# Kernel optimization log

Hardware: AMD Instinct MI355X
Metric: run time of the kernel (lower is better)

Reference implementation:

```python
import jax, jax.numpy as jnp
from jax import lax
import numpy as np

B, S, G = 16, 384, 384
N = S + G
E_CHAR, D = 100, 128
H = D // 2              # LSTM hidden per direction
NHEAD, NHID = 4, 64
T = 21                  # crf_input_dim = label_alphabet.size() + 1
START, STOP = T - 2, T - 1
ALPHA = 0.2
CHAR_V, GAZ_V = 8000, 100000
NEG = -9e15             # pyGAT masked_fill value


def setup_inputs():
    key = jax.random.key(0)
    ks = jax.random.split(key, 20)
    f32 = jnp.float32
    def nrm(k, shape, s=0.05):
        return (jax.random.normal(k, shape) * s).astype(f32)
    eye = jnp.eye(N, dtype=bool)
    def adj(k):
        return ((jax.random.uniform(k, (B, N, N)) < 0.1) | eye[None]).astype(jnp.int32)
    return dict(
        batch_char=jax.random.randint(ks[0], (B, S), 0, CHAR_V),
        batch_len=jnp.full((B,), S, jnp.int32),
        gaz_list=jax.random.randint(ks[1], (B, G), 0, GAZ_V),
        t_graph=adj(ks[2]), c_graph=adj(ks[3]), l_graph=adj(ks[4]),
        mask=jnp.ones((B, S), jnp.int32),
        char_table=nrm(ks[5], (CHAR_V, E_CHAR)),
        gaz_table=nrm(ks[6], (GAZ_V, D)),
        w_ih_f=nrm(ks[7], (4 * H, E_CHAR)), w_hh_f=nrm(ks[8], (4 * H, H)),
        b_f=jnp.zeros((4 * H,), f32),
        w_ih_b=nrm(ks[9], (4 * H, E_CHAR)), w_hh_b=nrm(ks[10], (4 * H, H)),
        b_b=jnp.zeros((4 * H,), f32),
        h2h_W=nrm(ks[11], (T, D)), h2h_b=jnp.zeros((T,), f32),
        gat_Wh=nrm(ks[12], (3, NHEAD, D, NHID)),
        gat_ah=nrm(ks[13], (3, NHEAD, 2 * NHID)),
        gat_Wo=nrm(ks[14], (3, NHEAD * NHID, T)),
        gat_ao=nrm(ks[15], (3, 2 * T)),
        fuse_w=jnp.ones((4,), f32),
        transitions=nrm(ks[16], (T, T)),
    )


def _lstm_dir(x, w_ih, w_hh, b, reverse):
    # x: [B,S,E]; torch gate order i,f,g,o
    Bb = x.shape[0]
    Hh = w_hh.shape[1]
    xw = jnp.einsum('bse,ge->bsg', x, w_ih) + b
    def step(carry, xt):
        h, c = carry
        g = xt + h @ w_hh.T
        i, f, gg, o = jnp.split(g, 4, axis=-1)
        c = jax.nn.sigmoid(f) * c + jax.nn.sigmoid(i) * jnp.tanh(gg)
        h = jax.nn.sigmoid(o) * jnp.tanh(c)
        return (h, c), h
    h0 = jnp.zeros((Bb, Hh), x.dtype)
    _, hs = lax.scan(step, (h0, h0), xw.swapaxes(0, 1), reverse=reverse)
    return hs.swapaxes(0, 1)


def _gat_layer(x, adj, W, a, concat):
    # pyGAT batched layer: e_ij = LeakyReLU(a . [Wh_i || Wh_j]), masked softmax over j
    h = jnp.einsum('bnd,df->bnf', x, W)
    F_ = W.shape[1]
    f1 = h @ a[:F_]           # [B,N]
    f2 = h @ a[F_:]
    e = jax.nn.leaky_relu(f1[:, :, None] + f2[:, None, :], negative_slope=ALPHA)
    e = jnp.where(adj > 0, e, NEG)
    att = jax.nn.softmax(e, axis=-1)
    out = jnp.einsum('bij,bjf->bif', att, h)
    return jax.nn.elu(out) if concat else out


def _gat(x, adj, Wh, ah, Wo, ao):
    heads = jax.vmap(lambda W, a: _gat_layer(x, adj, W, a, True))(Wh, ah)  # [H,B,N,F]
    hcat = jnp.moveaxis(heads, 0, 2).reshape(x.shape[0], x.shape[1], -1)
    return jax.nn.elu(_gat_layer(hcat, adj, Wo, ao, False))


def _crf_feature(batch_char, gaz_list, graphs, char_table, gaz_table,
                 w_ih_f, w_hh_f, b_f, w_ih_b, w_hh_b, b_b, h2h_W, h2h_b,
                 gat_Wh, gat_ah, gat_Wo, gat_ao, fuse_w):
    emb = char_table[batch_char]                      # [B,S,E_CHAR]
    hf = _lstm_dir(emb, w_ih_f, w_hh_f, b_f, False)
    hb = _lstm_dir(emb, w_ih_b, w_hh_b, b_b, True)
    lstm_feat = jnp.concatenate([hf, hb], axis=-1)    # [B,S,D]
    gaz_feat = gaz_table[gaz_list]                    # [B,G,D]
    gat_in = jnp.concatenate([lstm_feat, gaz_feat], axis=1)  # [B,N,D]
    gat_outs = [_gat(gat_in, adj, gat_Wh[k], gat_ah[k], gat_Wo[k], gat_ao[k])[:, :S]
                for k, adj in enumerate(graphs)]
    lstm_proj = lstm_feat @ h2h_W.T + h2h_b           # [B,S,T]
    return (fuse_w[0] * lstm_proj + fuse_w[1] * gat_outs[0]
            + fuse_w[2] * gat_outs[1] + fuse_w[3] * gat_outs[2])


def _viterbi(feats, transitions, mask):
    Bb, Ss, Tt = feats.shape
    ids = jnp.arange(Tt)
    part0 = feats[:, 0, :] + transitions[START][None, :]
    def step(part, inp):
        feat_t, m_t = inp
        cur = part[:, :, None] + transitions[None] + feat_t[:, None, :]  # [B,prev,cur]
        new = cur.max(axis=1)
        bp = cur.argmax(axis=1)
        m = (m_t > 0)[:, None]
        return jnp.where(m, new, part), jnp.where(m, bp, ids[None, :])
    part, bps = lax.scan(step, part0,
                         (feats[:, 1:].swapaxes(0, 1), mask[:, 1:].swapaxes(0, 1)))
    last_tag = jnp.argmax(part + transitions[:, STOP][None, :], axis=1)
    def back(tag, bp):
        prev = jnp.take_along_axis(bp, tag[:, None], axis=1)[:, 0]
        return prev, prev
    _, prevs = lax.scan(back, last_tag, bps, reverse=True)   # prevs[j] = tag at time j
    return jnp.concatenate([prevs.swapaxes(0, 1), last_tag[:, None]], axis=1)


def reference(batch_char, batch_len, gaz_list, t_graph, c_graph, l_graph, mask,
              char_table, gaz_table, w_ih_f, w_hh_f, b_f, w_ih_b, w_hh_b, b_b,
              h2h_W, h2h_b, gat_Wh, gat_ah, gat_Wo, gat_ao, fuse_w, transitions):
    # batch_len is all == S (mask all ones), so packed BiLSTM == plain BiLSTM
    feats = _crf_feature(batch_char, gaz_list, (t_graph, c_graph, l_graph),
                         char_table, gaz_table, w_ih_f, w_hh_f, b_f,
                         w_ih_b, w_hh_b, b_b, h2h_W, h2h_b,
                         gat_Wh, gat_ah, gat_Wo, gat_ao, fuse_w)
    return _viterbi(feats, transitions, mask)
```

## Files before the change

kernel.cpp:

```cpp
#include <hip/hip_runtime.h>
#include <hip/hip_bf16.h>
#include <cstdint>
#include <cstddef>

#define BB 16
#define SS 384
#define GG 384
#define NN 768
#define DD 128
#define EC 100
#define TT 21
#define NHEADS 4
#define BN (BB*NN)
#define BS (BB*SS)

typedef float v2f __attribute__((ext_vector_type(2)));

__device__ __forceinline__ float sigf(float x) { return 1.0f / (1.0f + __expf(-x)); }
__device__ __forceinline__ float tanh_fast(float x) {
    return 1.0f - 2.0f / (__expf(2.0f * x) + 1.0f);
}
__device__ __forceinline__ float wred_max(float v) {
    #pragma unroll
    for (int o = 32; o > 0; o >>= 1) v = fmaxf(v, __shfl_xor(v, o));
    return v;
}
__device__ __forceinline__ float wred_sum(float v) {
    #pragma unroll
    for (int o = 32; o > 0; o >>= 1) v += __shfl_xor(v, o);
    return v;
}

__global__ __launch_bounds__(256) void k_xw(
    const int* __restrict__ batch_char, const float* __restrict__ char_table,
    const float* __restrict__ w_ih_f, const float* __restrict__ b_f,
    const float* __restrict__ w_ih_b, const float* __restrict__ b_b,
    float* __restrict__ xw_f, float* __restrict__ xw_b)
{
    __shared__ float At[EC * 68];
    __shared__ float Bt[EC * 68];
    __shared__ int   chs[64];
    const int tid = threadIdx.x;
    const int rt  = blockIdx.x;
    const int ot  = blockIdx.y;
    const int dir = ot >> 2, gt = ot & 3;
    const float* wih  = dir ? w_ih_b : w_ih_f;
    const float* bias = dir ? b_b    : b_f;
    float*       out  = dir ? xw_b   : xw_f;

    if (tid < 64) chs[tid] = batch_char[rt * 64 + tid];
    __syncthreads();
    for (int idx = tid; idx < 64 * EC; idx += 256) {
        int r = idx / EC, e = idx - r * EC;
        At[e * 68 + r] = char_table[(size_t)chs[r] * EC + e];
        Bt[e * 68 + r] = wih[(size_t)(gt * 64 + r) * EC + e];
    }
    __syncthreads();

    const int ty = tid >> 4, tx = tid & 15;
    const int r0 = ty * 4, c0 = tx * 4;
    float acc[4][4] = {};
    #pragma unroll 4
    for (int e = 0; e < EC; ++e) {
        float4 a = *(const float4*)&At[e * 68 + r0];
        float4 bv = *(const float4*)&Bt[e * 68 + c0];
        float av[4] = {a.x, a.y, a.z, a.w};
        float bb[4] = {bv.x, bv.y, bv.z, bv.w};
        #pragma unroll
        for (int i = 0; i < 4; ++i)
            #pragma unroll
            for (int j = 0; j < 4; ++j) acc[i][j] = fmaf(av[i], bb[j], acc[i][j]);
    }
    #pragma unroll
    for (int i = 0; i < 4; ++i) {
        int row = rt * 64 + r0 + i;
        int gc  = gt * 64 + c0;
        float4 o;
        o.x = acc[i][0] + bias[gc + 0];
        o.y = acc[i][1] + bias[gc + 1];
        o.z = acc[i][2] + bias[gc + 2];
        o.w = acc[i][3] + bias[gc + 3];
        *(float4*)&out[(size_t)row * 256 + gc] = o;
    }
}

__global__ __launch_bounds__(256) void k_gaz(
    const int* __restrict__ gaz_list, const float* __restrict__ gaz_table,
    float* __restrict__ gat_in)
{
    int idx = blockIdx.x * 256 + threadIdx.x;
    int d = idx & 127;
    int rest = idx >> 7;
    int g = rest % GG;
    int b = rest / GG;
    float v = gaz_table[(size_t)gaz_list[b * GG + g] * DD + d];
    gat_in[((size_t)b * NN + SS + g) * DD + d] = v;
}

__global__ __launch_bounds__(256) void k_lstm(
    const float* __restrict__ xw_f, const float* __restrict__ xw_b,
    const float* __restrict__ w_hh_f, const float* __restrict__ w_hh_b,
    float* __restrict__ gat_in)
{
    __shared__ float part[2][4][64][4];
    __shared__ float hbuf[4][64];
    const int tid = threadIdx.x, wv = tid >> 6, lane = tid & 63;
    const int b = blockIdx.x >> 1, dir = blockIdx.x & 1;
    const float* xw  = (dir ? xw_b : xw_f) + (size_t)b * SS * 256;
    const float* whh = dir ? w_hh_b : w_hh_f;
    v2f w2[4][8];
    #pragma unroll
    for (int g4 = 0; g4 < 4; ++g4) {
        const float* r = whh + (size_t)(g4 * 64 + lane) * 64 + 16 * wv;
        #pragma unroll
        for (int jj = 0; jj < 8; ++jj) w2[g4][jj] = v2f{r[2 * jj], r[2 * jj + 1]};
    }
    hbuf[wv][lane] = 0.f;
    float c = 0.f;
    int buf = 0;
    const int t0 = dir ? (SS - 1) : 0;
    float x0 = xw[t0 * 256 +   0 + lane];
    float x1 = xw[t0 * 256 +  64 + lane];
    float x2 = xw[t0 * 256 + 128 + lane];
    float x3 = xw[t0 * 256 + 192 + lane];
    const v2f* h2p = (const v2f*)&hbuf[wv][16 * wv];
    for (int tt = 0; tt < SS; ++tt) {
        const int t = dir ? (SS - 1 - tt) : tt;
        const int tn = dir ? (t - 1) : (t + 1);
        v2f a0 = v2f{0.f, 0.f}, a1 = v2f{0.f, 0.f}, a2 = v2f{0.f, 0.f}, a3 = v2f{0.f, 0.f};
        #pragma unroll
        for (int jj = 0; jj < 8; ++jj) {
            v2f hv = h2p[jj];
            a0 = __builtin_elementwise_fma(hv, w2[0][jj], a0);
            a1 = __builtin_elementwise_fma(hv, w2[1][jj], a1);
            a2 = __builtin_elementwise_fma(hv, w2[2][jj], a2);
            a3 = __builtin_elementwise_fma(hv, w2[3][jj], a3);
        }
        float4 pw;
        pw.x = a0.x + a0.y; pw.y = a1.x + a1.y;
        pw.z = a2.x + a2.y; pw.w = a3.x + a3.y;
        *(float4*)part[buf][wv][lane] = pw;
        float nx0 = 0.f, nx1 = 0.f, nx2 = 0.f, nx3 = 0.f;
        if (tt + 1 < SS) {
            nx0 = xw[tn * 256 +   0 + lane];
            nx1 = xw[tn * 256 +  64 + lane];
            nx2 = xw[tn * 256 + 128 + lane];
            nx3 = xw[tn * 256 + 192 + lane];
        }
        __syncthreads();
        float4 p0 = *(const float4*)part[buf][0][lane];
        float4 p1 = *(const float4*)part[buf][1][lane];
        float4 p2 = *(const float4*)part[buf][2][lane];
        float4 p3 = *(const float4*)part[buf][3][lane];
        float gi = ((p0.x + p1.x) + (p2.x + p3.x)) + x0;
        float gf = ((p0.y + p1.y) + (p2.y + p3.y)) + x1;
        float gg = ((p0.z + p1.z) + (p2.z + p3.z)) + x2;
        float go = ((p0.w + p1.w) + (p2.w + p3.w)) + x3;
        float nc = sigf(gf) * c + sigf(gi) * tanh_fast(gg);
        float nh = sigf(go) * tanh_fast(nc);
        c = nc;
        hbuf[wv][lane] = nh;
        if (wv == 0) gat_in[((size_t)b * NN + t) * DD + dir * 64 + lane] = nh;
        x0 = nx0; x1 = nx1; x2 = nx2; x3 = nx3;
        buf ^= 1;
    }
}

__global__ __launch_bounds__(256) void k_p1(
    const float* __restrict__ gat_in, const float* __restrict__ gat_Wh,
    const float* __restrict__ gat_ah, int k,
    float* __restrict__ h1, float* __restrict__ f1g, float* __restrict__ f2g)
{
    __shared__ float At[64 * 68];
    __shared__ float Bt[64 * 68];
    __shared__ float sf1[64], sf2[64];
    const int tid = threadIdx.x;
    const int rt = blockIdx.x, hd = blockIdx.y;
    if (tid < 64) { sf1[tid] = 0.f; sf2[tid] = 0.f; }
    const float* W = gat_Wh + ((size_t)(k * NHEADS + hd)) * DD * 64;
    const int ty = tid >> 4, tx = tid & 15;
    const int r0 = ty * 4, c0 = tx * 4;
    float acc[4][4] = {};
    for (int ph = 0; ph < 2; ++ph) {
        __syncthreads();
        for (int idx = tid; idx < 64 * 64; idx += 256) {
            int r = idx >> 6, e = idx & 63;
            At[e * 68 + r] = gat_in[((size_t)(rt * 64 + r)) * DD + ph * 64 + e];
            Bt[e * 68 + r] = W[(size_t)(ph * 64 + e) * 64 + r];
        }
        __syncthreads();
        #pragma unroll 4
        for (int e = 0; e < 64; ++e) {
            float4 a = *(const float4*)&At[e * 68 + r0];
            float4 bv = *(const float4*)&Bt[e * 68 + c0];
            float av[4] = {a.x, a.y, a.z, a.w};
            float bb[4] = {bv.x, bv.y, bv.z, bv.w};
            #pragma unroll
            for (int i = 0; i < 4; ++i)
                #pragma unroll
                for (int j = 0; j < 4; ++j) acc[i][j] = fmaf(av[i], bb[j], acc[i][j]);
        }
    }
    const float* ah = gat_ah + (size_t)(k * NHEADS + hd) * 128;
    float a1[4], a2[4];
    #pragma unroll
    for (int j = 0; j < 4; ++j) { a1[j] = ah[c0 + j]; a2[j] = ah[64 + c0 + j]; }
    #pragma unroll
    for (int i = 0; i < 4; ++i) {
        int n = rt * 64 + r0 + i;
        float4 o = make_float4(acc[i][0], acc[i][1], acc[i][2], acc[i][3]);
        *(float4*)&h1[((size_t)n * NHEADS + hd) * 64 + c0] = o;
        float p1 = acc[i][0] * a1[0] + acc[i][1] * a1[1] + acc[i][2] * a1[2] + acc[i][3] * a1[3];
        float p2 = acc[i][0] * a2[0] + acc[i][1] * a2[1] + acc[i][2] * a2[2] + acc[i][3] * a2[3];
        atomicAdd(&sf1[r0 + i], p1);
        atomicAdd(&sf2[r0 + i], p2);
    }
    __syncthreads();
    if (tid < 64) {
        f1g[hd * BN + rt * 64 + tid] = sf1[tid];
        f2g[hd * BN + rt * 64 + tid] = sf2[tid];
    }
}

__global__ __launch_bounds__(256) void k_attn1(
    const int* __restrict__ adj, const float* __restrict__ h1,
    const float* __restrict__ f1g, const float* __restrict__ f2g,
    float* __restrict__ out1, unsigned long long* __restrict__ packed)
{
    __shared__ int   nbr[NN];
    __shared__ float ep[NHEADS][NN];
    __shared__ unsigned long long wm[12];
    __shared__ int cntS;
    const int tid = threadIdx.x, wave = tid >> 6, lane = tid & 63;
    const int n = blockIdx.x;
    const int b = n / NN;
    #pragma unroll
    for (int it = 0; it < 3; ++it) {
        int j = it * 256 + tid;
        int a = adj[(size_t)n * NN + j];
        unsigned long long m = __ballot(a > 0);
        if (lane == 0) { wm[it * 4 + wave] = m; packed[(size_t)n * 12 + it * 4 + wave] = m; }
    }
    __syncthreads();
    if (wave == 0) {
        unsigned long long m = (lane < 12) ? wm[lane] : 0ULL;
        int pc = __popcll(m);
        int inc = pc;
        #pragma unroll
        for (int d = 1; d < 16; d <<= 1) { int t = __shfl_up(inc, d); if (lane >= d) inc += t; }
        int C = __shfl(inc, 11);
        if (lane == 0) cntS = C;
        int off = inc - pc;
        while (m) {
            int bit = __builtin_ctzll(m);
            nbr[off++] = lane * 64 + bit;
            m &= m - 1;
        }
    }
    __syncthreads();
    const int C = cntS;
    const int hd = wave;
    const float f1 = f1g[hd * BN + n];
    const float* f2p = f2g + hd * BN + b * NN;
    float mx = -3.0e38f;
    for (int t = lane; t < C; t += 64) {
        float e = f1 + f2p[nbr[t]];
        e = (e >= 0.f) ? e : 0.2f * e;
        ep[hd][t] = e;
        mx = fmaxf(mx, e);
    }
    mx = wred_max(mx);
    float sum = 0.f;
    for (int t = lane; t < C; t += 64) {
        float p = __expf(ep[hd][t] - mx);
        ep[hd][t] = p;
        sum += p;
    }
    sum = wred_sum(sum);
    const float* hb = h1 + (size_t)b * NN * (NHEADS * 64) + hd * 64 + lane;
    float ac0 = 0.f, ac1 = 0.f, ac2 = 0.f, ac3 = 0.f;
    int t = 0;
    for (; t + 3 < C; t += 4) {
        int j0 = nbr[t], j1 = nbr[t + 1], j2 = nbr[t + 2], j3 = nbr[t + 3];
        float p0 = ep[hd][t], p1 = ep[hd][t + 1], p2 = ep[hd][t + 2], p3 = ep[hd][t + 3];
        ac0 = fmaf(p0, hb[(size_t)j0 * 256], ac0);
        ac1 = fmaf(p1, hb[(size_t)j1 * 256], ac1);
        ac2 = fmaf(p2, hb[(size_t)j2 * 256], ac2);
        ac3 = fmaf(p3, hb[(size_t)j3 * 256], ac3);
    }
    for (; t < C; ++t) ac0 = fmaf(ep[hd][t], hb[(size_t)nbr[t] * 256], ac0);
    float r = ((ac0 + ac1) + (ac2 + ac3)) / sum;
    r = (r > 0.f) ? r : expm1f(r);
    out1[(size_t)n * 256 + hd * 64 + lane] = r;
}

__global__ __launch_bounds__(256) void k_p2(
    const float* __restrict__ out1, const float* __restrict__ gat_Wo,
    const float* __restrict__ gat_ao, int k,
    float* __restrict__ h2, float* __restrict__ f1o, float* __restrict__ f2o)
{
    __shared__ float ld[12 * 256];
    __shared__ float lf1[12], lf2[12];
    const int tid = threadIdx.x;
    const int blk = blockIdx.x;
    if (tid < 12) { lf1[tid] = 0.f; lf2[tid] = 0.f; }
    for (int idx = tid; idx < 12 * 256; idx += 256)
        ld[idx] = out1[(size_t)blk * 12 * 256 + idx];
    __syncthreads();
    if (tid < 252) {
        const int r = tid / TT, c = tid - r * TT;
        const float* Wo = gat_Wo + (size_t)k * 256 * TT;
        const float4* row4 = (const float4*)&ld[r * 256];
        float acc = 0.f;
        #pragma unroll 8
        for (int q4 = 0; q4 < 64; ++q4) {
            float4 v = row4[q4];
            int q = q4 * 4;
            acc = fmaf(v.x, Wo[(q + 0) * TT + c], acc);
            acc = fmaf(v.y, Wo[(q + 1) * TT + c], acc);
            acc = fmaf(v.z, Wo[(q + 2) * TT + c], acc);
            acc = fmaf(v.w, Wo[(q + 3) * TT + c], acc);
        }
        const int n = blk * 12 + r;
        h2[(size_t)n * TT + c] = acc;
        const float* ao = gat_ao + k * 2 * TT;
        atomicAdd(&lf1[r], acc * ao[c]);
        atomicAdd(&lf2[r], acc * ao[TT + c]);
    }
    __syncthreads();
    if (tid < 12) {
        f1o[blk * 12 + tid] = lf1[tid];
        f2o[blk * 12 + tid] = lf2[tid];
    }
}

__global__ __launch_bounds__(64) void k_attn2(
    const unsigned long long* __restrict__ packed,
    const float* __restrict__ h2, const float* __restrict__ f1o,
    const float* __restrict__ f2o, float* __restrict__ out2k)
{
    __shared__ int   nbr[NN];
    __shared__ float ep[NN];
    const int lane = threadIdx.x;
    const int blk = blockIdx.x;
    const int b = blk / SS, s = blk - b * SS;
    const int n = b * NN + s;
    unsigned long long w64 = (lane < 12) ? packed[(size_t)n * 12 + lane] : 0ULL;
    int pc = __popcll(w64);
    int inc = pc;
    #pragma unroll
    for (int d = 1; d < 16; d <<= 1) {
        int t = __shfl_up(inc, d, 16);
        if ((lane & 15) >= d) inc += t;
    }
    const int C = __shfl(inc, 11);
    int off = inc - pc;
    while (w64) {
        int bit = __builtin_ctzll(w64);
        nbr[off++] = lane * 64 + bit;
        w64 &= w64 - 1;
    }
    __syncthreads();
    const float f1 = f1o[n];
    const float* f2p = f2o + b * NN;
    float mx = -3.0e38f;
    for (int t = lane; t < C; t += 64) {
        int j = nbr[t];
        float e = f1 + f2p[j];
        e = (e >= 0.f) ? e : 0.2f * e;
        ep[t] = e;
        mx = fmaxf(mx, e);
    }
    mx = wred_max(mx);
    float sum = 0.f;
    for (int t = lane; t < C; t += 64) {
        float p = __expf(ep[t] - mx);
        ep[t] = p;
        sum += p;
    }
    sum = wred_sum(sum);
    const float* h2b = h2 + (size_t)b * NN * TT + ((lane < TT) ? lane : 0);
    float ac0 = 0.f, ac1 = 0.f, ac2 = 0.f, ac3 = 0.f;
    int t = 0;
    for (; t + 3 < C; t += 4) {
        int j0 = nbr[t], j1 = nbr[t + 1], j2 = nbr[t + 2], j3 = nbr[t + 3];
        float p0 = ep[t], p1 = ep[t + 1], p2 = ep[t + 2], p3 = ep[t + 3];
        ac0 = fmaf(p0, h2b[(size_t)j0 * TT], ac0);
        ac1 = fmaf(p1, h2b[(size_t)j1 * TT], ac1);
        ac2 = fmaf(p2, h2b[(size_t)j2 * TT], ac2);
        ac3 = fmaf(p3, h2b[(size_t)j3 * TT], ac3);
    }
    for (; t < C; ++t) ac0 = fmaf(ep[t], h2b[(size_t)nbr[t] * TT], ac0);
    if (lane < TT) {
        float r = ((ac0 + ac1) + (ac2 + ac3)) / sum;
        r = (r > 0.f) ? r : expm1f(r);
        out2k[(size_t)blk * TT + lane] = r;
    }
}

__global__ __launch_bounds__(64) void k_fuse(
    const float* __restrict__ gat_in, const float* __restrict__ h2h_W,
    const float* __restrict__ h2h_b, const float* __restrict__ fuse_w,
    const float* __restrict__ out2, float* __restrict__ feats)
{
    __shared__ float row[DD];
    const int lane = threadIdx.x;
    const int blk = blockIdx.x;
    const int b = blk / SS, s = blk - b * SS;
    const float* src = gat_in + ((size_t)b * NN + s) * DD;
    row[lane] = src[lane];
    row[lane + 64] = src[lane + 64];
    __syncthreads();
    if (lane < TT) {
        float acc = h2h_b[lane];
        const float4* w4 = (const float4*)&h2h_W[lane * DD];
        const float4* r4 = (const float4*)row;
        #pragma unroll 8
        for (int d4 = 0; d4 < 32; ++d4) {
            float4 w = w4[d4]; float4 v = r4[d4];
            acc = fmaf(w.x, v.x, acc); acc = fmaf(w.y, v.y, acc);
            acc = fmaf(w.z, v.z, acc); acc = fmaf(w.w, v.w, acc);
        }
        size_t o = (size_t)blk * TT + lane;
        feats[o] = fuse_w[0] * acc + fuse_w[1] * out2[o]
                 + fuse_w[2] * out2[(size_t)BS * TT + o]
                 + fuse_w[3] * out2[2 * (size_t)BS * TT + o];
    }
}

__global__ __launch_bounds__(64) void k_vit(
    const float* __restrict__ feats, const float* __restrict__ trans,
    int* __restrict__ out)
{
    __shared__ float part[24];
    __shared__ unsigned char bp[SS - 1][24];
    const int lane = threadIdx.x;
    const int b = blockIdx.x;
    const int pg = lane / TT;
    const int c = lane - pg * TT;
    const bool act = (pg < 3);
    const int p0 = pg * 7;
    float tc[7];
    if (act) {
        #pragma unroll
        for (int u = 0; u < 7; ++u) tc[u] = trans[(p0 + u) * TT + c];
    }
    if (lane < TT) part[lane] = feats[((size_t)b * SS) * TT + lane] + trans[19 * TT + lane];
    if (lane >= TT && lane < 24) part[lane] = -3.0e38f;
    __syncthreads();
    for (int t = 1; t < SS; ++t) {
        float best = -3.0e38f; int bi = 0;
        if (act) {
            #pragma unroll
            for (int u = 0; u < 7; ++u) {
                float v = part[p0 + u] + tc[u];
                if (v > best) { best = v; bi = p0 + u; }
            }
        }
        float bv1 = __shfl(best, lane + 21);
        int   bi1 = __shfl(bi,   lane + 21);
        float bv2 = __shfl(best, lane + 42);
        int   bi2 = __shfl(bi,   lane + 42);
        if (lane < TT) {
            if (bv1 > best) { best = bv1; bi = bi1; }
            if (bv2 > best) { best = bv2; bi = bi2; }
            bp[t - 1][lane] = (unsigned char)bi;
            part[lane] = best + feats[((size_t)b * SS + t) * TT + lane];
        }
        __syncthreads();
    }
    float fv = (lane < TT) ? part[lane] + trans[lane * TT + 20] : -3.0e38f;
    int fi = (lane < TT) ? lane : 0;
    #pragma unroll
    for (int o = 32; o > 0; o >>= 1) {
        float ov = __shfl_xor(fv, o);
        int oi = __shfl_xor(fi, o);
        if (ov > fv || (ov == fv && oi < fi)) { fv = ov; fi = oi; }
    }
    __syncthreads();
    if (lane == 0) {
        int cur = fi;
        out[b * SS + SS - 1] = cur;
        for (int u = SS - 2; u >= 0; --u) {
            cur = bp[u][cur];
            out[b * SS + u] = cur;
        }
    }
}

extern "C" void kernel_launch(void* const* d_in, const int* in_sizes, int n_in,
                              void* d_out, int out_size, void* d_ws, size_t ws_size,
                              hipStream_t stream) {
    (void)in_sizes; (void)n_in; (void)out_size; (void)ws_size;
    const int*   batch_char = (const int*)d_in[0];
    const int*   gaz_list   = (const int*)d_in[2];
    const int*   graphs[3]  = {(const int*)d_in[3], (const int*)d_in[4], (const int*)d_in[5]};
    const float* char_table = (const float*)d_in[7];
    const float* gaz_table  = (const float*)d_in[8];
    const float* w_ih_f = (const float*)d_in[9];
    const float* w_hh_f = (const float*)d_in[10];
    const float* b_f    = (const float*)d_in[11];
    const float* w_ih_b = (const float*)d_in[12];
    const float* w_hh_b = (const float*)d_in[13];
    const float* b_b    = (const float*)d_in[14];
    const float* h2h_W  = (const float*)d_in[15];
    const float* h2h_b  = (const float*)d_in[16];
    const float* gat_Wh = (const float*)d_in[17];
    const float* gat_ah = (const float*)d_in[18];
    const float* gat_Wo = (const float*)d_in[19];
    const float* gat_ao = (const float*)d_in[20];
    const float* fuse_w = (const float*)d_in[21];
    const float* trans  = (const float*)d_in[22];

    float* ws = (float*)d_ws;
    float* gat_in = ws;
    float* xw_f   = gat_in + 1572864;
    float* xw_b   = xw_f   + 1572864;
    float* h1     = xw_b   + 1572864;
    float* out1   = h1     + 3145728;
    float* h2     = out1   + 3145728;
    float* f1g    = h2     + 258048;
    float* f2g    = f1g    + 49152;
    float* f1o    = f2g    + 49152;
    float* f2o    = f1o    + 12288;
    float* out2   = f2o    + 12288;
    float* feats  = out2   + 387072;
    unsigned long long* packed = (unsigned long long*)(feats + 129024);

    k_xw<<<dim3(96, 8), 256, 0, stream>>>(batch_char, char_table, w_ih_f, b_f,
                                          w_ih_b, b_b, xw_f, xw_b);
    k_gaz<<<3072, 256, 0, stream>>>(gaz_list, gaz_table, gat_in);
    k_lstm<<<32, 256, 0, stream>>>(xw_f, xw_b, w_hh_f, w_hh_b, gat_in);
    for (int k = 0; k < 3; ++k) {
        k_p1<<<dim3(192, 4), 256, 0, stream>>>(gat_in, gat_Wh, gat_ah, k, h1, f1g, f2g);
        k_attn1<<<BN, 256, 0, stream>>>(graphs[k], h1, f1g, f2g, out1, packed);
        k_p2<<<1024, 256, 0, stream>>>(out1, gat_Wo, gat_ao, k, h2, f1o, f2o);
        k_attn2<<<BS, 64, 0, stream>>>(packed, h2, f1o, f2o, out2 + (size_t)k * BS * TT);
    }
    k_fuse<<<BS, 64, 0, stream>>>(gat_in, h2h_W, h2h_b, fuse_w, out2, feats);
    k_vit<<<BB, 64, 0, stream>>>(feats, trans, (int*)d_out);
}
```

Measured before the change: 949.3 us.

## Run each LSTM direction in a single wavefront to drop block barriers

The recurrent LSTM kernel moves from four waves, each computing a partial dot product over 16 hidden units, to one 64-lane wave per (batch, direction) that holds a full row of the recurrent weights in registers. This removes the per-timestep __syncthreads, the shared-memory partial-sum buffer and the cross-wave reduction on the serial critical path. In exchange each lane does four times more FMAs per step and keeps 256 weight floats in registers, which launch_bounds(64,1) is meant to allow. It also relies on in-order LDS access within one wavefront instead of a barrier between the write and read of hbuf.

After: 1.112 ms. +17.1%, slower.

```diff
diff --git a/kernel.cpp b/kernel.cpp
--- a/kernel.cpp
+++ b/kernel.cpp
@@ -97,49 +97,51 @@
     gat_in[((size_t)b * NN + SS + g) * DD + d] = v;
 }
 
-__global__ __launch_bounds__(256) void k_lstm(
+__global__ __launch_bounds__(64, 1) void k_lstm(
     const float* __restrict__ xw_f, const float* __restrict__ xw_b,
     const float* __restrict__ w_hh_f, const float* __restrict__ w_hh_b,
     float* __restrict__ gat_in)
 {
-    __shared__ float part[2][4][64][4];
-    __shared__ float hbuf[4][64];
-    const int tid = threadIdx.x, wv = tid >> 6, lane = tid & 63;
+    __shared__ float hbuf[64];
+    const int lane = threadIdx.x;
     const int b = blockIdx.x >> 1, dir = blockIdx.x & 1;
     const float* xw  = (dir ? xw_b : xw_f) + (size_t)b * SS * 256;
     const float* whh = dir ? w_hh_b : w_hh_f;
-    v2f w2[4][8];
-    #pragma unroll
-    for (int g4 = 0; g4 < 4; ++g4) {
-        const float* r = whh + (size_t)(g4 * 64 + lane) * 64 + 16 * wv;
+    v2f w2[4][32];
+    #pragma unroll
+    for (int g = 0; g < 4; ++g) {
+        const float* r = whh + (size_t)(g * 64 + lane) * 64;
         #pragma unroll
-        for (int jj = 0; jj < 8; ++jj) w2[g4][jj] = v2f{r[2 * jj], r[2 * jj + 1]};
-    }
-    hbuf[wv][lane] = 0.f;
+        for (int q = 0; q < 16; ++q) {
+            float4 v = *(const float4*)&r[4 * q];
+            w2[g][2 * q + 0] = v2f{v.x, v.y};
+            w2[g][2 * q + 1] = v2f{v.z, v.w};
+        }
+    }
+    hbuf[lane] = 0.f;
     float c = 0.f;
-    int buf = 0;
     const int t0 = dir ? (SS - 1) : 0;
     float x0 = xw[t0 * 256 +   0 + lane];
     float x1 = xw[t0 * 256 +  64 + lane];
     float x2 = xw[t0 * 256 + 128 + lane];
     float x3 = xw[t0 * 256 + 192 + lane];
-    const v2f* h2p = (const v2f*)&hbuf[wv][16 * wv];
+    const v2f* h2p = (const v2f*)hbuf;
     for (int tt = 0; tt < SS; ++tt) {
         const int t = dir ? (SS - 1 - tt) : tt;
         const int tn = dir ? (t - 1) : (t + 1);
         v2f a0 = v2f{0.f, 0.f}, a1 = v2f{0.f, 0.f}, a2 = v2f{0.f, 0.f}, a3 = v2f{0.f, 0.f};
         #pragma unroll
-        for (int jj = 0; jj < 8; ++jj) {
+        for (int jj = 0; jj < 32; ++jj) {
             v2f hv = h2p[jj];
             a0 = __builtin_elementwise_fma(hv, w2[0][jj], a0);
             a1 = __builtin_elementwise_fma(hv, w2[1][jj], a1);
             a2 = __builtin_elementwise_fma(hv, w2[2][jj], a2);
             a3 = __builtin_elementwise_fma(hv, w2[3][jj], a3);
         }
-        float4 pw;
-        pw.x = a0.x + a0.y; pw.y = a1.x + a1.y;
-        pw.z = a2.x + a2.y; pw.w = a3.x + a3.y;
-        *(float4*)part[buf][wv][lane] = pw;
+        float gi = x0 + a0.x + a0.y;
+        float gf = x1 + a1.x + a1.y;
+        float gg = x2 + a2.x + a2.y;
+        float go = x3 + a3.x + a3.y;
         float nx0 = 0.f, nx1 = 0.f, nx2 = 0.f, nx3 = 0.f;
         if (tt + 1 < SS) {
             nx0 = xw[tn * 256 +   0 + lane];
@@ -147,22 +149,12 @@
             nx2 = xw[tn * 256 + 128 + lane];
             nx3 = xw[tn * 256 + 192 + lane];
         }
-        __syncthreads();
-        float4 p0 = *(const float4*)part[buf][0][lane];
-        float4 p1 = *(const float4*)part[buf][1][lane];
-        float4 p2 = *(const float4*)part[buf][2][lane];
-        float4 p3 = *(const float4*)part[buf][3][lane];
-        float gi = ((p0.x + p1.x) + (p2.x + p3.x)) + x0;
-        float gf = ((p0.y + p1.y) + (p2.y + p3.y)) + x1;
-        float gg = ((p0.z + p1.z) + (p2.z + p3.z)) + x2;
-        float go = ((p0.w + p1.w) + (p2.w + p3.w)) + x3;
         float nc = sigf(gf) * c + sigf(gi) * tanh_fast(gg);
         float nh = sigf(go) * tanh_fast(nc);
         c = nc;
-        hbuf[wv][lane] = nh;
-        if (wv == 0) gat_in[((size_t)b * NN + t) * DD + dir * 64 + lane] = nh;
+        hbuf[lane] = nh;
+        gat_in[((size_t)b * NN + t) * DD + dir * 64 + lane] = nh;
         x0 = nx0; x1 = nx1; x2 = nx2; x3 = nx3;
-        buf ^= 1;
     }
 }
 
@@ -530,7 +522,7 @@
     k_xw<<<dim3(96, 8), 256, 0, stream>>>(batch_char, char_table, w_ih_f, b_f,
                                           w_ih_b, b_b, xw_f, xw_b);
     k_gaz<<<3072, 256, 0, stream>>>(gaz_list, gaz_table, gat_in);
-    k_lstm<<<32, 256, 0, stream>>>(xw_f, xw_b, w_hh_f, w_hh_b, gat_in);
+    k_lstm<<<32, 64, 0, stream>>>(xw_f, xw_b, w_hh_f, w_hh_b, gat_in);
     for (int k = 0; k < 3; ++k) {
         k_p1<<<dim3(192, 4), 256, 0, stream>>>(gat_in, gat_Wh, gat_ah, k, h1, f1g, f2g);
         k_attn1<<<BN, 256, 0, stream>>>(graphs[k], h1, f1g, f2g, out1, packed);
```

## Halve LSTM waves per block and make Viterbi barrier-free with register state

Applied to the files above, without the earlier changes.

The LSTM recurrence now runs with two waves per block, each holding half of W_hh in registers, which halves the cross-wave reduction and barrier cost per timestep. The Viterbi kernel preloads the whole emission sequence into shared memory and keeps the partition scores in registers, exchanged with shuffles. This removes the per-step __syncthreads and global loads. The backtrace also uses shuffles with prefetched backpointers instead of serial shared reads. The risk is more register pressure in the LSTM and a longer FMA chain per wave.

New measurement: 1.002 ms. 1.06x slower.

```diff
diff --git a/kernel.cpp b/kernel.cpp
--- a/kernel.cpp
+++ b/kernel.cpp
@@ -97,23 +97,27 @@
     gat_in[((size_t)b * NN + SS + g) * DD + d] = v;
 }
 
-__global__ __launch_bounds__(256) void k_lstm(
+__global__ __launch_bounds__(128, 1) void k_lstm(
     const float* __restrict__ xw_f, const float* __restrict__ xw_b,
     const float* __restrict__ w_hh_f, const float* __restrict__ w_hh_b,
     float* __restrict__ gat_in)
 {
-    __shared__ float part[2][4][64][4];
-    __shared__ float hbuf[4][64];
+    __shared__ float part[2][2][64][4];
+    __shared__ float hbuf[2][64];
     const int tid = threadIdx.x, wv = tid >> 6, lane = tid & 63;
     const int b = blockIdx.x >> 1, dir = blockIdx.x & 1;
     const float* xw  = (dir ? xw_b : xw_f) + (size_t)b * SS * 256;
     const float* whh = dir ? w_hh_b : w_hh_f;
-    v2f w2[4][8];
-    #pragma unroll
-    for (int g4 = 0; g4 < 4; ++g4) {
-        const float* r = whh + (size_t)(g4 * 64 + lane) * 64 + 16 * wv;
-        #pragma unroll
-        for (int jj = 0; jj < 8; ++jj) w2[g4][jj] = v2f{r[2 * jj], r[2 * jj + 1]};
+    v2f w2[4][16];
+    #pragma unroll
+    for (int g = 0; g < 4; ++g) {
+        const float* r = whh + (size_t)(g * 64 + lane) * 64 + 32 * wv;
+        #pragma unroll
+        for (int q = 0; q < 8; ++q) {
+            float4 v = *(const float4*)&r[4 * q];
+            w2[g][2 * q + 0] = v2f{v.x, v.y};
+            w2[g][2 * q + 1] = v2f{v.z, v.w};
+        }
     }
     hbuf[wv][lane] = 0.f;
     float c = 0.f;
@@ -123,13 +127,13 @@
     float x1 = xw[t0 * 256 +  64 + lane];
     float x2 = xw[t0 * 256 + 128 + lane];
     float x3 = xw[t0 * 256 + 192 + lane];
-    const v2f* h2p = (const v2f*)&hbuf[wv][16 * wv];
+    const v2f* h2p = (const v2f*)&hbuf[wv][32 * wv];
     for (int tt = 0; tt < SS; ++tt) {
         const int t = dir ? (SS - 1 - tt) : tt;
         const int tn = dir ? (t - 1) : (t + 1);
         v2f a0 = v2f{0.f, 0.f}, a1 = v2f{0.f, 0.f}, a2 = v2f{0.f, 0.f}, a3 = v2f{0.f, 0.f};
         #pragma unroll
-        for (int jj = 0; jj < 8; ++jj) {
+        for (int jj = 0; jj < 16; ++jj) {
             v2f hv = h2p[jj];
             a0 = __builtin_elementwise_fma(hv, w2[0][jj], a0);
             a1 = __builtin_elementwise_fma(hv, w2[1][jj], a1);
@@ -150,12 +154,10 @@
         __syncthreads();
         float4 p0 = *(const float4*)part[buf][0][lane];
         float4 p1 = *(const float4*)part[buf][1][lane];
-        float4 p2 = *(const float4*)part[buf][2][lane];
-        float4 p3 = *(const float4*)part[buf][3][lane];
-        float gi = ((p0.x + p1.x) + (p2.x + p3.x)) + x0;
-        float gf = ((p0.y + p1.y) + (p2.y + p3.y)) + x1;
-        float gg = ((p0.z + p1.z) + (p2.z + p3.z)) + x2;
-        float go = ((p0.w + p1.w) + (p2.w + p3.w)) + x3;
+        float gi = (p0.x + p1.x) + x0;
+        float gf = (p0.y + p1.y) + x1;
+        float gg = (p0.z + p1.z) + x2;
+        float go = (p0.w + p1.w) + x3;
         float nc = sigf(gf) * c + sigf(gi) * tanh_fast(gg);
         float nh = sigf(go) * tanh_fast(nc);
         c = nc;
@@ -428,14 +430,26 @@
     }
 }
 
-__global__ __launch_bounds__(64) void k_vit(
+__global__ __launch_bounds__(256) void k_vit(
     const float* __restrict__ feats, const float* __restrict__ trans,
     int* __restrict__ out)
 {
-    __shared__ float part[24];
-    __shared__ unsigned char bp[SS - 1][24];
-    const int lane = threadIdx.x;
+    __shared__ float sfeat[SS * TT];
+    __shared__ unsigned char bp[(SS - 1) * 24];
+    const int tid = threadIdx.x;
     const int b = blockIdx.x;
+    {
+        const float4* src = (const float4*)(feats + (size_t)b * SS * TT);
+        float4* dst = (float4*)sfeat;
+        #pragma unroll
+        for (int i = 0; i < 8; ++i) {
+            int idx = i * 256 + tid;
+            if (idx < 2016) dst[idx] = src[idx];
+        }
+    }
+    __syncthreads();
+    if (tid >= 64) return;
+    const int lane = tid;
     const int pg = lane / TT;
     const int c = lane - pg * TT;
     const bool act = (pg < 3);
@@ -445,17 +459,17 @@
         #pragma unroll
         for (int u = 0; u < 7; ++u) tc[u] = trans[(p0 + u) * TT + c];
     }
-    if (lane < TT) part[lane] = feats[((size_t)b * SS) * TT + lane] + trans[19 * TT + lane];
-    if (lane >= TT && lane < 24) part[lane] = -3.0e38f;
-    __syncthreads();
+    const float tr_stop = (lane < TT) ? trans[lane * TT + 20] : 0.f;
+    float pp = (lane < TT) ? (sfeat[lane] + trans[19 * TT + lane]) : -3.0e38f;
+    const int sfl = (lane < TT) ? lane : 0;
     for (int t = 1; t < SS; ++t) {
+        float sf = sfeat[t * TT + sfl];
         float best = -3.0e38f; int bi = 0;
-        if (act) {
-            #pragma unroll
-            for (int u = 0; u < 7; ++u) {
-                float v = part[p0 + u] + tc[u];
-                if (v > best) { best = v; bi = p0 + u; }
-            }
+        #pragma unroll
+        for (int u = 0; u < 7; ++u) {
+            float pu = __shfl(pp, p0 + u);
+            float v = pu + tc[u];
+            if (act && v > best) { best = v; bi = p0 + u; }
         }
         float bv1 = __shfl(best, lane + 21);
         int   bi1 = __shfl(bi,   lane + 21);
@@ -464,12 +478,11 @@
         if (lane < TT) {
             if (bv1 > best) { best = bv1; bi = bi1; }
             if (bv2 > best) { best = bv2; bi = bi2; }
-            bp[t - 1][lane] = (unsigned char)bi;
-            part[lane] = best + feats[((size_t)b * SS + t) * TT + lane];
-        }
-        __syncthreads();
-    }
-    float fv = (lane < TT) ? part[lane] + trans[lane * TT + 20] : -3.0e38f;
+            bp[(t - 1) * 24 + lane] = (unsigned char)bi;
+            pp = best + sf;
+        }
+    }
+    float fv = (lane < TT) ? pp + tr_stop : -3.0e38f;
     int fi = (lane < TT) ? lane : 0;
     #pragma unroll
     for (int o = 32; o > 0; o >>= 1) {
@@ -477,14 +490,15 @@
         int oi = __shfl_xor(fi, o);
         if (ov > fv || (ov == fv && oi < fi)) { fv = ov; fi = oi; }
     }
-    __syncthreads();
-    if (lane == 0) {
-        int cur = fi;
-        out[b * SS + SS - 1] = cur;
-        for (int u = SS - 2; u >= 0; --u) {
-            cur = bp[u][cur];
-            out[b * SS + u] = cur;
-        }
+    int cur = fi;
+    if (lane == 0) out[b * SS + SS - 1] = cur;
+    int r = (lane < TT) ? (int)bp[(SS - 2) * 24 + lane] : 0;
+    for (int u = SS - 2; u >= 0; --u) {
+        int rn = 0;
+        if (u > 0 && lane < TT) rn = (int)bp[(u - 1) * 24 + lane];
+        cur = __shfl(r, cur);
+        if (lane == 0) out[b * SS + u] = cur;
+        r = rn;
     }
 }
 
@@ -530,7 +544,7 @@
     k_xw<<<dim3(96, 8), 256, 0, stream>>>(batch_char, char_table, w_ih_f, b_f,
                                           w_ih_b, b_b, xw_f, xw_b);
     k_gaz<<<3072, 256, 0, stream>>>(gaz_list, gaz_table, gat_in);
-    k_lstm<<<32, 256, 0, stream>>>(xw_f, xw_b, w_hh_f, w_hh_b, gat_in);
+    k_lstm<<<32, 128, 0, stream>>>(xw_f, xw_b, w_hh_f, w_hh_b, gat_in);
     for (int k = 0; k < 3; ++k) {
         k_p1<<<dim3(192, 4), 256, 0, stream>>>(gat_in, gat_Wh, gat_ah, k, h1, f1g, f2g);
         k_attn1<<<BN, 256, 0, stream>>>(graphs[k], h1, f1g, f2g, out1, packed);
@@ -538,5 +552,5 @@
         k_attn2<<<BS, 64, 0, stream>>>(packed, h2, f1o, f2o, out2 + (size_t)k * BS * TT);
     }
     k_fuse<<<BS, 64, 0, stream>>>(gat_in, h2h_W, h2h_b, fuse_w, out2, feats);
-    k_vit<<<BB, 64, 0, stream>>>(feats, trans, (int*)d_out);
-}
+    k_vit<<<BB, 256, 0, stream>>>(feats, trans, (int*)d_out);
+}
```
